# Performance work log

Measured on AMD Instinct MI355X. Metric: run time of the kernel, lower is better.

The kernel has to match this reference:

```python
import jax, jax.numpy as jnp
import numpy as np

GAMMA = 1.0
DICE_EPS = 1.0


def setup_inputs() -> dict:
    key = jax.random.key(0)
    k1, k2, k3 = jax.random.split(key, 3)
    B, N, C = 32, 16384, 50
    predictions = jax.random.normal(k1, (B, N, C), dtype=jnp.float32)
    targets = jax.random.randint(k2, (B, N), 0, C, dtype=jnp.int64)
    pred_choice = jax.random.randint(k3, (B, N), 0, C, dtype=jnp.int64)
    return {"predictions": predictions, "targets": targets, "pred_choice": pred_choice}


def reference(predictions, targets, pred_choice):
    # predictions: [B, N, C] logits; targets, pred_choice: [B, N] int labels
    logp = jax.nn.log_softmax(predictions, axis=-1)              # [B, N, C]
    logp_t = jnp.take_along_axis(logp, targets[..., None], axis=-1)[..., 0]  # [B, N]
    ce_loss = -jnp.mean(logp_t)                                   # scalar (CrossEntropyLoss mean)

    # focal modulation: pn = softmax prob of the true class; loss = mean((1-pn)^gamma) * ce
    pn = jnp.exp(logp_t)                                          # [B, N]
    loss = jnp.mean((1.0 - pn) ** GAMMA) * ce_loss

    # dice: the per-class loop in the original reduces exactly to
    # top = total correct predictions, bot = 2 * total points
    tf = targets.reshape(-1)
    pf = pred_choice.reshape(-1)
    top = jnp.sum((pf == tf).astype(jnp.float32))
    bot = jnp.float32(2 * tf.shape[0])
    dice_loss = 1.0 - 2.0 * (top + DICE_EPS) / (bot + DICE_EPS)

    return loss + dice_loss
```

## Files before the change

### kernel.cpp

```cpp
#include <hip/hip_runtime.h>
#include <math.h>


#define NCLS 50
#define BLK 256

__global__ __launch_bounds__(BLK) void pnloss_main(
    const float* __restrict__ pred,
    const int* __restrict__ targets,
    const int* __restrict__ pchoice,
    float4* __restrict__ partials,
    int rows)
{
    const int tid = threadIdx.x;
    const int row = blockIdx.x * BLK + tid;

    float logpt = 0.f, pn = 0.f, match = 0.f;

    if (row < rows) {
        const float2* rp = reinterpret_cast<const float2*>(pred + (size_t)row * NCLS);

        const int t  = targets[row];
        const int pc = pchoice[row];

        float2 v[NCLS / 2];
        #pragma unroll
        for (int j = 0; j < NCLS / 2; ++j) v[j] = rp[j];
        const float xt = pred[(size_t)row * NCLS + t];

        __builtin_amdgcn_sched_barrier(0);

        float s = 0.f;
        #pragma unroll
        for (int j = 0; j < NCLS / 2; ++j)
            s += __expf(v[j].x) + __expf(v[j].y);

        logpt = xt - __logf(s);
        pn    = __expf(logpt);
        match = (pc == t) ? 1.f : 0.f;
    }

    #pragma unroll
    for (int off = 32; off > 0; off >>= 1) {
        logpt += __shfl_down(logpt, off);
        pn    += __shfl_down(pn, off);
        match += __shfl_down(match, off);
    }

    __shared__ float sm[3][BLK / 64];
    const int wid  = tid >> 6;
    const int lane = tid & 63;
    if (lane == 0) { sm[0][wid] = logpt; sm[1][wid] = pn; sm[2][wid] = match; }
    __syncthreads();

    if (tid == 0) {
        float a = 0.f, b = 0.f, c = 0.f;
        #pragma unroll
        for (int w = 0; w < BLK / 64; ++w) { a += sm[0][w]; b += sm[1][w]; c += sm[2][w]; }
        partials[blockIdx.x] = make_float4(a, b, c, 0.f);
    }
}

__global__ __launch_bounds__(BLK) void pnloss_final(
    const float4* __restrict__ partials,
    int nblocks, float inv_rows, float two_rows,
    float* __restrict__ out)
{
    float a = 0.f, b = 0.f, c = 0.f;
    for (int i = threadIdx.x; i < nblocks; i += BLK) {
        const float4 p = partials[i];
        a += p.x; b += p.y; c += p.z;
    }

    #pragma unroll
    for (int off = 32; off > 0; off >>= 1) {
        a += __shfl_down(a, off);
        b += __shfl_down(b, off);
        c += __shfl_down(c, off);
    }

    __shared__ float sm[3][BLK / 64];
    const int wid  = threadIdx.x >> 6;
    const int lane = threadIdx.x & 63;
    if (lane == 0) { sm[0][wid] = a; sm[1][wid] = b; sm[2][wid] = c; }
    __syncthreads();

    if (threadIdx.x == 0) {
        float sa = 0.f, sb = 0.f, sc = 0.f;
        #pragma unroll
        for (int w = 0; w < BLK / 64; ++w) { sa += sm[0][w]; sb += sm[1][w]; sc += sm[2][w]; }
        const float ce    = -sa * inv_rows;
        const float focal = 1.f - sb * inv_rows;
        const float loss  = focal * ce;
        const float dice  = 1.f - 2.f * (sc + 1.f) / (two_rows + 1.f);
        out[0] = loss + dice;
    }
}

extern "C" void kernel_launch(void* const* d_in, const int* in_sizes, int n_in,
                              void* d_out, int out_size, void* d_ws, size_t ws_size,
                              hipStream_t stream) {
    const float* pred     = (const float*)d_in[0];
    const int*   targets  = (const int*)d_in[1];
    const int*   pchoice  = (const int*)d_in[2];
    float*       out      = (float*)d_out;
    float4*      partials = (float4*)d_ws;

    const int rows    = in_sizes[1];
    const int nblocks = (rows + BLK - 1) / BLK;

    pnloss_main<<<nblocks, BLK, 0, stream>>>(pred, targets, pchoice, partials, rows);
    pnloss_final<<<1, BLK, 0, stream>>>(partials, nblocks,
                                        1.0f / (float)rows, 2.0f * (float)rows, out);
}
```

Measured before the change: 25.58 us.

## Fuse final reduction into main kernel via atomics and last-block finalize

Replaces the two-kernel partials-then-final reduction with a single kernel where each block atomically adds its three sums into global accumulators and a ticket counter lets the last block compute the scalar output. A memset of the workspace is added before the launch. This is meant to remove the second kernel launch and its serialized tail, at the cost of 2048 blocks contending on three atomic addresses plus a memset operation in the stream.

```diff
diff --git a/kernel.cpp b/kernel.cpp
--- a/kernel.cpp
+++ b/kernel.cpp
@@ -5,12 +5,15 @@
 #define NCLS 50
 #define BLK 256
 
-__global__ __launch_bounds__(BLK) void pnloss_main(
+__global__ __launch_bounds__(BLK) void pnloss_fused(
     const float* __restrict__ pred,
     const int* __restrict__ targets,
     const int* __restrict__ pchoice,
-    float4* __restrict__ partials,
-    int rows)
+    float* __restrict__ acc,
+    unsigned int* __restrict__ counter,
+    int rows, int nblocks,
+    float inv_rows, float two_rows,
+    float* __restrict__ out)
 {
     const int tid = threadIdx.x;
     const int row = blockIdx.x * BLK + tid;
@@ -57,59 +60,42 @@
         float a = 0.f, b = 0.f, c = 0.f;
         #pragma unroll
         for (int w = 0; w < BLK / 64; ++w) { a += sm[0][w]; b += sm[1][w]; c += sm[2][w]; }
-        partials[blockIdx.x] = make_float4(a, b, c, 0.f);
-    }
-}
 
-__global__ __launch_bounds__(BLK) void pnloss_final(
-    const float4* __restrict__ partials,
-    int nblocks, float inv_rows, float two_rows,
-    float* __restrict__ out)
-{
-    float a = 0.f, b = 0.f, c = 0.f;
-    for (int i = threadIdx.x; i < nblocks; i += BLK) {
-        const float4 p = partials[i];
-        a += p.x; b += p.y; c += p.z;
-    }
+        atomicAdd(&acc[0],  a);
+        atomicAdd(&acc[16], b);
+        atomicAdd(&acc[32], c);
+        asm volatile("s_waitcnt vmcnt(0)" ::: "memory");
+        const unsigned int old = atomicAdd(counter, 1u);
 
-    #pragma unroll
-    for (int off = 32; off > 0; off >>= 1) {
-        a += __shfl_down(a, off);
-        b += __shfl_down(b, off);
-        c += __shfl_down(c, off);
-    }
-
-    __shared__ float sm[3][BLK / 64];
-    const int wid  = threadIdx.x >> 6;
-    const int lane = threadIdx.x & 63;
-    if (lane == 0) { sm[0][wid] = a; sm[1][wid] = b; sm[2][wid] = c; }
-    __syncthreads();
-
-    if (threadIdx.x == 0) {
-        float sa = 0.f, sb = 0.f, sc = 0.f;
-        #pragma unroll
-        for (int w = 0; w < BLK / 64; ++w) { sa += sm[0][w]; sb += sm[1][w]; sc += sm[2][w]; }
-        const float ce    = -sa * inv_rows;
-        const float focal = 1.f - sb * inv_rows;
-        const float loss  = focal * ce;
-        const float dice  = 1.f - 2.f * (sc + 1.f) / (two_rows + 1.f);
-        out[0] = loss + dice;
+        if (old == (unsigned int)(nblocks - 1)) {
+            const float sa = atomicAdd(&acc[0],  0.f);
+            const float sb = atomicAdd(&acc[16], 0.f);
+            const float sc = atomicAdd(&acc[32], 0.f);
+            const float ce    = -sa * inv_rows;
+            const float focal = 1.f - sb * inv_rows;
+            const float loss  = focal * ce;
+            const float dice  = 1.f - 2.f * (sc + 1.f) / (two_rows + 1.f);
+            out[0] = loss + dice;
+        }
     }
 }
 
 extern "C" void kernel_launch(void* const* d_in, const int* in_sizes, int n_in,
                               void* d_out, int out_size, void* d_ws, size_t ws_size,
                               hipStream_t stream) {
-    const float* pred     = (const float*)d_in[0];
-    const int*   targets  = (const int*)d_in[1];
-    const int*   pchoice  = (const int*)d_in[2];
-    float*       out      = (float*)d_out;
-    float4*      partials = (float4*)d_ws;
+    const float* pred    = (const float*)d_in[0];
+    const int*   targets = (const int*)d_in[1];
+    const int*   pchoice = (const int*)d_in[2];
+    float*       out     = (float*)d_out;
+
+    float*        acc     = (float*)d_ws;
+    unsigned int* counter = (unsigned int*)((char*)d_ws + 192);
 
     const int rows    = in_sizes[1];
     const int nblocks = (rows + BLK - 1) / BLK;
 
-    pnloss_main<<<nblocks, BLK, 0, stream>>>(pred, targets, pchoice, partials, rows);
-    pnloss_final<<<1, BLK, 0, stream>>>(partials, nblocks,
-                                        1.0f / (float)rows, 2.0f * (float)rows, out);
+    hipMemsetAsync(d_ws, 0, 256, stream);
+    pnloss_fused<<<nblocks, BLK, 0, stream>>>(pred, targets, pchoice,
+                                              acc, counter, rows, nblocks,
+                                              1.0f / (float)rows, 2.0f * (float)rows, out);
 }
```

Result: slower. 63.90 us (+149.9%).
